# Performance work log

Hardware: AMD Instinct MI355X
Metric: run time of the kernel (lower is better)

Reference implementation:

```python
import jax, jax.numpy as jnp
import numpy as np

# dims (match init_kwargs)
N, M = 128, 2048
DX, DY, DU, DZ = 64, 8, 256, 256
EPS = 0.01


def setup_inputs() -> dict:
    key = jax.random.key(0)
    kit = iter(jax.random.split(key, 40))
    def w(*shape):
        fan_in = shape[-1]
        return jax.random.normal(next(kit), shape, jnp.float32) / np.float32(np.sqrt(fan_in))
    def b(*shape):
        return 0.1 * jax.random.normal(next(kit), shape, jnp.float32)
    inp = {
        'X_tensor': jax.random.normal(next(kit), (N, DX), jnp.float32),
        'U_tensor': jax.random.normal(next(kit), (M, DY), jnp.float32),
        'Y_tensor': jax.random.normal(next(kit), (N, DY), jnp.float32),
        # context path (x -> u_i)
        'Wt0': w(DU, DX), 'bt0': b(DU),
        'Wt1': w(DU, DU), 'bt1': b(DU),
        # PICNN cell 0 (input cell, no z term)
        'Wyu0': w(DY, DX), 'byu0': b(DY), 'Wy0': w(DZ, DY), 'Wu0': w(DZ, DX), 'b0': b(DZ),
        # PICNN cell 1 (hidden cell, nonneg Wz1 via softplus)
        'Wzu1': w(DZ, DU), 'bzu1': b(DZ), 'Wz1': w(DZ, DZ),
        'Wyu1': w(DY, DU), 'byu1': b(DY), 'Wy1': w(DZ, DY), 'Wu1': w(DZ, DU), 'b1': b(DZ),
        # PICNN cell 2 (output cell, scalar potential)
        'Wzu2': w(DZ, DU), 'bzu2': b(DZ), 'Wz2': w(1, DZ),
        'Wyu2': w(DY, DU), 'byu2': b(DY), 'Wy2': w(1, DY), 'Wu2': w(1, DU), 'b2': b(1),
    }
    return inp


def _psi(X, U, Y, Wt0, bt0, Wt1, bt1, Wyu0, byu0, Wy0, Wu0, b0,
         Wzu1, bzu1, Wz1, Wyu1, byu1, Wy1, Wu1, b1,
         Wzu2, bzu2, Wz2, Wyu2, byu2, Wy2, Wu2, b2):
    relu = jax.nn.relu
    # context path depends only on X -> compute once per row, broadcast over m samples
    u1 = relu(X @ Wt0.T + bt0)                       # [n, du]
    u2 = relu(u1 @ Wt1.T + bt1)                      # [n, du]
    # cell 0: z1 [n, m, dz]  (pairwise over X rows x U samples)
    gy0 = X @ Wyu0.T + byu0                          # [n, dy]
    z1 = relu(jnp.einsum('md,nd,zd->nmz', U, gy0, Wy0)
              + (X @ Wu0.T + b0)[:, None, :])
    # cell 1: hidden convex cell with nonneg z-weight
    gz1 = relu(u1 @ Wzu1.T + bzu1)                   # [n, dz]
    gy1 = u1 @ Wyu1.T + byu1                         # [n, dy]
    z2 = relu(jnp.einsum('nmz,nz,kz->nmk', z1, gz1, jax.nn.softplus(Wz1))
              + jnp.einsum('md,nd,kd->nmk', U, gy1, Wy1)
              + (u1 @ Wu1.T + b1)[:, None, :])       # [n, m, dz]
    # output cell -> scalar potential phi(x_i, u_j)
    gz2 = relu(u2 @ Wzu2.T + bzu2)                   # [n, dz]
    gy2 = u2 @ Wyu2.T + byu2                         # [n, dy]
    phi = (jnp.einsum('nmz,nz,z->nm', z2, gz2, jax.nn.softplus(Wz2)[0])
           + jnp.einsum('md,nd,d->nm', U, gy2, Wy2[0])
           + (u2 @ Wu2[0] + b2[0])[:, None])         # [n, m]
    # entropic OT dual psi with stable row-wise logsumexp
    cost = Y @ U.T                                   # [n, m]
    slack = cost - phi
    row_max = jnp.max(slack, axis=1, keepdims=True)
    log_mean_exp = (jax.nn.logsumexp((slack - row_max) / EPS, axis=1, keepdims=True)
                    - jnp.log(jnp.float32(slack.shape[1])))
    return EPS * (log_mean_exp + row_max / EPS)      # [n, 1]


def reference(X_tensor, U_tensor, Y_tensor, Wt0, bt0, Wt1, bt1, Wyu0, byu0, Wy0, Wu0, b0,
              Wzu1, bzu1, Wz1, Wyu1, byu1, Wy1, Wu1, b1,
              Wzu2, bzu2, Wz2, Wyu2, byu2, Wy2, Wu2, b2):
    return _psi(X_tensor, U_tensor, Y_tensor, Wt0, bt0, Wt1, bt1, Wyu0, byu0, Wy0, Wu0, b0,
                Wzu1, bzu1, Wz1, Wyu1, byu1, Wy1, Wu1, b1,
                Wzu2, bzu2, Wz2, Wyu2, byu2, Wy2, Wu2, b2)
```

## Files before the change

kernel.cpp:

```cpp
#include <hip/hip_runtime.h>

#define NN 128
#define MM 2048
#define EPSF 0.01f

typedef __bf16 bf16x8 __attribute__((ext_vector_type(8)));
typedef __bf16 bf16x4 __attribute__((ext_vector_type(4)));
typedef float  f32x4  __attribute__((ext_vector_type(4)));

#define WS_SLACK 0
#define WS_W2    262144
#define WS_GZ1   294912
#define WS_YV    327680
#define WS_CU2   328704
#define WS_WTF   328832
#define WS_A2    361600
#define WS_B2    394368
#define WS_BX    918656

__device__ __forceinline__ float softplusf(float x) {
    return x > 20.f ? x : log1pf(expf(x));
}

__device__ __forceinline__ bf16x8 ld_cvt8(const float* __restrict__ p) {
    const float4* p4 = (const float4*)p;
    float4 a = p4[0], b = p4[1];
    bf16x8 r;
    r[0] = (__bf16)a.x; r[1] = (__bf16)a.y; r[2] = (__bf16)a.z; r[3] = (__bf16)a.w;
    r[4] = (__bf16)b.x; r[5] = (__bf16)b.y; r[6] = (__bf16)b.z; r[7] = (__bf16)b.w;
    return r;
}

__global__ __launch_bounds__(256) void k_ctx3(
    const float* __restrict__ X, const float* __restrict__ Y,
    const float* __restrict__ U,
    const float* __restrict__ Wt0, const float* __restrict__ bt0,
    const float* __restrict__ Wt1, const float* __restrict__ bt1,
    const float* __restrict__ Wyu0, const float* __restrict__ byu0,
    const float* __restrict__ Wy0,
    const float* __restrict__ Wu0, const float* __restrict__ b0,
    const float* __restrict__ Wzu1, const float* __restrict__ bzu1,
    const float* __restrict__ Wz1,
    const float* __restrict__ Wyu1, const float* __restrict__ byu1,
    const float* __restrict__ Wy1,
    const float* __restrict__ Wu1, const float* __restrict__ b1,
    const float* __restrict__ Wzu2, const float* __restrict__ bzu2,
    const float* __restrict__ Wz2,
    const float* __restrict__ Wyu2, const float* __restrict__ byu2,
    const float* __restrict__ Wy2,
    const float* __restrict__ Wu2, const float* __restrict__ b2,
    float* __restrict__ ws)
{
    __shared__ __bf16 u1b[16][264];
    __shared__ __bf16 u2b[16][264];
    __shared__ __bf16 c0q[16][64];
    __shared__ __bf16 c1q[16][64];
    __shared__ float gy0s[16][8];
    __shared__ float gy1s[16][8];

    const int t = threadIdx.x, b = blockIdx.x;
    const int w = t >> 6, lane = t & 63;
    const int c = lane & 15, q = lane >> 4;
    const int g = b >> 2, s = b & 3;
    const int nb = g * 16;

#pragma unroll
    for (int jj = 0; jj < 2; ++jj) {
        const int o = (b * 512 + jj * 256 + t) * 4;
        const int j0 = o & 7;
        const int cc = (o >> 3) & 15;
        const int qq = (o >> 7) & 3;
        const int ch = (o >> 9) & 7;
        const int kt = o >> 12;
        const float* src = Wz1 + (kt * 16 + cc) * 256 + ch * 32 + qq * 8 + j0;
        float4 v = *(const float4*)src;
        bf16x4 r;
        r[0] = (__bf16)softplusf(v.x); r[1] = (__bf16)softplusf(v.y);
        r[2] = (__bf16)softplusf(v.z); r[3] = (__bf16)softplusf(v.w);
        *(bf16x4*)((__bf16*)(ws + WS_WTF) + o) = r;
    }
#pragma unroll
    for (int j = 0; j < 8; ++j) {
        const int i = b * 2048 + j * 256 + t;
        const int m = i >> 5, cc = i & 31;
        float v = cc < 8 ? U[m * 8 + cc] : (cc == 8 ? 1.f : 0.f);
        ((__bf16*)(ws + WS_A2))[i] = (__bf16)v;
    }

    bf16x8 a1[2];
#pragma unroll
    for (int ch = 0; ch < 2; ++ch)
        a1[ch] = ld_cvt8(X + (nb + c) * 64 + ch * 32 + q * 8);

    for (int tt = w; tt < 16; tt += 4) {
        const int col = tt * 16 + c;
        const float* rp = Wt0 + col * 64;
        f32x4 D = {0.f, 0.f, 0.f, 0.f};
#pragma unroll
        for (int ch = 0; ch < 2; ++ch) {
            bf16x8 bb = ld_cvt8(rp + ch * 32 + q * 8);
            D = __builtin_amdgcn_mfma_f32_16x16x32_bf16(a1[ch], bb, D, 0, 0, 0);
        }
        const float bv = bt0[col];
#pragma unroll
        for (int r = 0; r < 4; ++r)
            u1b[4 * q + r][col] = (__bf16)fmaxf(D[r] + bv, 0.f);
    }
    {
        const int col = (4 * s + w) * 16 + c;
        const float* rp = Wu0 + col * 64;
        f32x4 D = {0.f, 0.f, 0.f, 0.f};
#pragma unroll
        for (int ch = 0; ch < 2; ++ch) {
            bf16x8 bb = ld_cvt8(rp + ch * 32 + q * 8);
            D = __builtin_amdgcn_mfma_f32_16x16x32_bf16(a1[ch], bb, D, 0, 0, 0);
        }
        const float bv = b0[col];
#pragma unroll
        for (int r = 0; r < 4; ++r)
            c0q[4 * q + r][w * 16 + c] = (__bf16)(D[r] + bv);
    }
    if (w == 0) {
        const float* rp = Wyu0 + (c & 7) * 64;
        f32x4 D = {0.f, 0.f, 0.f, 0.f};
#pragma unroll
        for (int ch = 0; ch < 2; ++ch) {
            bf16x8 bb = ld_cvt8(rp + ch * 32 + q * 8);
            D = __builtin_amdgcn_mfma_f32_16x16x32_bf16(a1[ch], bb, D, 0, 0, 0);
        }
        if (c < 8) {
            const float bv = byu0[c];
#pragma unroll
            for (int r = 0; r < 4; ++r)
                gy0s[4 * q + r][c] = D[r] + bv;
        }
    }
    __syncthreads();

    bf16x8 aF[8];
#pragma unroll
    for (int ch = 0; ch < 8; ++ch)
        aF[ch] = *(const bf16x8*)&u1b[c][ch * 32 + q * 8];

    for (int tt = w; tt < 16; tt += 4) {
        const int col = tt * 16 + c;
        const float* rp = Wt1 + col * 256;
        f32x4 D = {0.f, 0.f, 0.f, 0.f};
#pragma unroll
        for (int ch = 0; ch < 8; ++ch) {
            bf16x8 bb = ld_cvt8(rp + ch * 32 + q * 8);
            D = __builtin_amdgcn_mfma_f32_16x16x32_bf16(aF[ch], bb, D, 0, 0, 0);
        }
        const float bv = bt1[col];
#pragma unroll
        for (int r = 0; r < 4; ++r)
            u2b[4 * q + r][col] = (__bf16)fmaxf(D[r] + bv, 0.f);
    }
    {
        const int col = (4 * s + w) * 16 + c;
        const float* rp = Wzu1 + col * 256;
        f32x4 D = {0.f, 0.f, 0.f, 0.f};
#pragma unroll
        for (int ch = 0; ch < 8; ++ch) {
            bf16x8 bb = ld_cvt8(rp + ch * 32 + q * 8);
            D = __builtin_amdgcn_mfma_f32_16x16x32_bf16(aF[ch], bb, D, 0, 0, 0);
        }
        const float bv = bzu1[col];
#pragma unroll
        for (int r = 0; r < 4; ++r)
            ws[WS_GZ1 + (nb + 4 * q + r) * 256 + col] = fmaxf(D[r] + bv, 0.f);
    }
    {
        const int col = (4 * s + w) * 16 + c;
        const float* rp = Wu1 + col * 256;
        f32x4 D = {0.f, 0.f, 0.f, 0.f};
#pragma unroll
        for (int ch = 0; ch < 8; ++ch) {
            bf16x8 bb = ld_cvt8(rp + ch * 32 + q * 8);
            D = __builtin_amdgcn_mfma_f32_16x16x32_bf16(aF[ch], bb, D, 0, 0, 0);
        }
        const float bv = b1[col];
#pragma unroll
        for (int r = 0; r < 4; ++r)
            c1q[4 * q + r][w * 16 + c] = (__bf16)(D[r] + bv);
    }
    if (w == 0) {
        const float* rp = Wyu1 + (c & 7) * 256;
        f32x4 D = {0.f, 0.f, 0.f, 0.f};
#pragma unroll
        for (int ch = 0; ch < 8; ++ch) {
            bf16x8 bb = ld_cvt8(rp + ch * 32 + q * 8);
            D = __builtin_amdgcn_mfma_f32_16x16x32_bf16(aF[ch], bb, D, 0, 0, 0);
        }
        if (c < 8) {
            const float bv = byu1[c];
#pragma unroll
            for (int r = 0; r < 4; ++r)
                gy1s[4 * q + r][c] = D[r] + bv;
        }
    }
    __syncthreads();

    bf16x8 aG[8];
#pragma unroll
    for (int ch = 0; ch < 8; ++ch)
        aG[ch] = *(const bf16x8*)&u2b[c][ch * 32 + q * 8];

    {
        const int col = (4 * s + w) * 16 + c;
        const float* rp = Wzu2 + col * 256;
        f32x4 D = {0.f, 0.f, 0.f, 0.f};
#pragma unroll
        for (int ch = 0; ch < 8; ++ch) {
            bf16x8 bb = ld_cvt8(rp + ch * 32 + q * 8);
            D = __builtin_amdgcn_mfma_f32_16x16x32_bf16(aG[ch], bb, D, 0, 0, 0);
        }
        const float bv = bzu2[col];
        const float sp = softplusf(Wz2[col]);
#pragma unroll
        for (int r = 0; r < 4; ++r) {
            float gz2 = fmaxf(D[r] + bv, 0.f);
            ws[WS_W2 + (nb + 4 * q + r) * 256 + col] = gz2 * sp;
        }
    }
    if (s == 0 && w == 0) {
        const float* rp = (c < 8) ? (Wyu2 + c * 256) : Wu2;
        f32x4 D = {0.f, 0.f, 0.f, 0.f};
#pragma unroll
        for (int ch = 0; ch < 8; ++ch) {
            bf16x8 bb = ld_cvt8(rp + ch * 32 + q * 8);
            D = __builtin_amdgcn_mfma_f32_16x16x32_bf16(aG[ch], bb, D, 0, 0, 0);
        }
        if (c < 8) {
            const float bv = byu2[c];
            const float wy2 = Wy2[c];
#pragma unroll
            for (int r = 0; r < 4; ++r) {
                const int n = nb + 4 * q + r;
                ws[WS_YV + n * 8 + c] = Y[n * 8 + c] - (D[r] + bv) * wy2;
            }
        } else if (c == 8) {
#pragma unroll
            for (int r = 0; r < 4; ++r)
                ws[WS_CU2 + nb + 4 * q + r] = D[r] + b2[0];
        }
    }

    bf16x8 zz;
#pragma unroll
    for (int j = 0; j < 8; ++j) zz[j] = (__bf16)0.f;
#pragma unroll
    for (int j = 0; j < 4; ++j) {
        const int idx = j * 256 + t;
        const int zl = idx & 63, nl = idx >> 6;
        const int z = 64 * s + zl, n = nb + nl;
        {
            const float* wy = Wy0 + z * 8;
            __bf16* dst = (__bf16*)(ws + WS_B2) + (n * 256 + z) * 32;
            bf16x8 v0, v1 = zz;
#pragma unroll
            for (int d = 0; d < 8; ++d) v0[d] = (__bf16)(gy0s[nl][d] * wy[d]);
            v1[0] = c0q[nl][zl];
            *(bf16x8*)(dst)      = v0;
            *(bf16x8*)(dst + 8)  = v1;
            *(bf16x8*)(dst + 16) = zz;
            *(bf16x8*)(dst + 24) = zz;
        }
        {
            const float* wy = Wy1 + z * 8;
            __bf16* dst = (__bf16*)(ws + WS_BX) + (n * 256 + z) * 32;
            bf16x8 v0, v1 = zz;
#pragma unroll
            for (int d = 0; d < 8; ++d) v0[d] = (__bf16)(gy1s[nl][d] * wy[d]);
            v1[0] = c1q[nl][zl];
            *(bf16x8*)(dst)      = v0;
            *(bf16x8*)(dst + 8)  = v1;
            *(bf16x8*)(dst + 16) = zz;
            *(bf16x8*)(dst + 24) = zz;
        }
    }
}

__global__ __launch_bounds__(256, 4) void k_main(
    const float* __restrict__ U,
    float* __restrict__ ws)
{
    __shared__ __bf16 zh[64][264];
    __shared__ float gz1s[256];
    __shared__ float w2s[256];
    __shared__ float sdot[64];
    __shared__ float psum[4][64];

    const int t  = threadIdx.x;
    const int n  = blockIdx.y;
    const int m0 = blockIdx.x * 64;
    const int w    = t >> 6;
    const int lane = t & 63;
    const int c = lane & 15;
    const int q = lane >> 4;

    gz1s[t] = ws[WS_GZ1 + n * 256 + t];
    w2s[t]  = ws[WS_W2  + n * 256 + t];
    if (t < 64) {
        float sd = 0.f;
#pragma unroll
        for (int d = 0; d < 8; ++d)
            sd += U[(m0 + t) * 8 + d] * ws[WS_YV + n * 8 + d];
        sdot[t] = sd;
    }

    const __bf16* A2p = (const __bf16*)(ws + WS_A2);
    const __bf16* B2p = (const __bf16*)(ws + WS_B2) + n * 8192;
    const __bf16* BXp = (const __bf16*)(ws + WS_BX) + n * 8192;
    const __bf16* WTF = (const __bf16*)(ws + WS_WTF);

    bf16x8 a2f[4];
#pragma unroll
    for (int mi = 0; mi < 4; ++mi)
        a2f[mi] = *(const bf16x8*)(A2p + (m0 + 16 * mi + c) * 32 + q * 8);

    {
        bf16x8 b2f[4];
#pragma unroll
        for (int zt = 0; zt < 4; ++zt)
            b2f[zt] = *(const bf16x8*)(B2p + (64 * w + 16 * zt + c) * 32 + q * 8);
        f32x4 pre[4][4];
#pragma unroll
        for (int zt = 0; zt < 4; ++zt)
#pragma unroll
            for (int mi = 0; mi < 4; ++mi) {
                f32x4 zacc = {0.f, 0.f, 0.f, 0.f};
                pre[zt][mi] = __builtin_amdgcn_mfma_f32_16x16x32_bf16(
                    b2f[zt], a2f[mi], zacc, 0, 0, 0);
            }
#pragma unroll
        for (int zt = 0; zt < 4; ++zt) {
            const int zb = 64 * w + 16 * zt + 4 * q;
#pragma unroll
            for (int mi = 0; mi < 4; ++mi) {
                bf16x4 v4;
#pragma unroll
                for (int r = 0; r < 4; ++r)
                    v4[r] = (__bf16)(fmaxf(pre[zt][mi][r], 0.f) * gz1s[zb + r]);
                *(bf16x4*)&zh[c + 16 * mi][zb] = v4;
            }
        }
    }

    f32x4 acc[4][4];
#pragma unroll
    for (int mi = 0; mi < 4; ++mi)
#pragma unroll
        for (int kj = 0; kj < 4; ++kj)
            acc[mi][kj] = f32x4{0.f, 0.f, 0.f, 0.f};

    __syncthreads();

    for (int ch = 0; ch < 8; ++ch) {
        bf16x8 az[4], bw[4];
#pragma unroll
        for (int mi = 0; mi < 4; ++mi)
            az[mi] = *(const bf16x8*)&zh[c + 16 * mi][ch * 32 + q * 8];
#pragma unroll
        for (int kj = 0; kj < 4; ++kj)
            bw[kj] = *(const bf16x8*)(WTF + ((4 * w + kj) * 8 + ch) * 512 + lane * 8);
#pragma unroll
        for (int mi = 0; mi < 4; ++mi)
#pragma unroll
            for (int kj = 0; kj < 4; ++kj)
                acc[mi][kj] = __builtin_amdgcn_mfma_f32_16x16x32_bf16(
                    az[mi], bw[kj], acc[mi][kj], 0, 0, 0);
    }
    {
        bf16x8 bx[4];
#pragma unroll
        for (int kj = 0; kj < 4; ++kj)
            bx[kj] = *(const bf16x8*)(BXp + (64 * w + 16 * kj + c) * 32 + q * 8);
#pragma unroll
        for (int mi = 0; mi < 4; ++mi)
#pragma unroll
            for (int kj = 0; kj < 4; ++kj)
                acc[mi][kj] = __builtin_amdgcn_mfma_f32_16x16x32_bf16(
                    a2f[mi], bx[kj], acc[mi][kj], 0, 0, 0);
    }

    float p[4][4];
#pragma unroll
    for (int mi = 0; mi < 4; ++mi)
#pragma unroll
        for (int r = 0; r < 4; ++r) p[mi][r] = 0.f;
#pragma unroll
    for (int kj = 0; kj < 4; ++kj) {
        float w2v = w2s[64 * w + 16 * kj + c];
#pragma unroll
        for (int mi = 0; mi < 4; ++mi)
#pragma unroll
            for (int r = 0; r < 4; ++r)
                p[mi][r] += fmaxf(acc[mi][kj][r], 0.f) * w2v;
    }
#pragma unroll
    for (int mi = 0; mi < 4; ++mi)
#pragma unroll
        for (int r = 0; r < 4; ++r) {
            float v = p[mi][r];
            v += __shfl_xor(v, 8);
            v += __shfl_xor(v, 4);
            v += __shfl_xor(v, 2);
            v += __shfl_xor(v, 1);
            p[mi][r] = v;
        }
    if (c == 0) {
#pragma unroll
        for (int mi = 0; mi < 4; ++mi)
            *(float4*)&psum[w][16 * mi + 4 * q] =
                make_float4(p[mi][0], p[mi][1], p[mi][2], p[mi][3]);
    }
    __syncthreads();
    if (t < 64) {
        float cu2 = ws[WS_CU2 + n];
        float pp = psum[0][t] + psum[1][t] + psum[2][t] + psum[3][t];
        ws[WS_SLACK + n * 2048 + m0 + t] = sdot[t] - cu2 - pp;
    }
}

__global__ __launch_bounds__(256) void k_lse(const float* __restrict__ ws,
                                             float* __restrict__ out) {
    __shared__ float redmax[4];
    __shared__ float redsum[4];
    const int n = blockIdx.x;
    const int t = threadIdx.x;
    const float* s = ws + WS_SLACK + n * 2048;

    float vals[8];
    float mx = -3.4e38f;
#pragma unroll
    for (int i = 0; i < 8; ++i) {
        vals[i] = s[t + 256 * i];
        mx = fmaxf(mx, vals[i]);
    }
#pragma unroll
    for (int off = 32; off; off >>= 1) mx = fmaxf(mx, __shfl_xor(mx, off));
    if ((t & 63) == 0) redmax[t >> 6] = mx;
    __syncthreads();
    mx = fmaxf(fmaxf(redmax[0], redmax[1]), fmaxf(redmax[2], redmax[3]));

    float sum = 0.f;
#pragma unroll
    for (int i = 0; i < 8; ++i) sum += expf((vals[i] - mx) * (1.f / EPSF));
#pragma unroll
    for (int off = 32; off; off >>= 1) sum += __shfl_xor(sum, off);
    if ((t & 63) == 0) redsum[t >> 6] = sum;
    __syncthreads();
    if (t == 0) {
        float S = redsum[0] + redsum[1] + redsum[2] + redsum[3];
        out[n] = EPSF * logf(S * (1.f / 2048.f)) + mx;
    }
}

extern "C" void kernel_launch(void* const* d_in, const int* in_sizes, int n_in,
                              void* d_out, int out_size, void* d_ws, size_t ws_size,
                              hipStream_t stream) {
    const float* X    = (const float*)d_in[0];
    const float* Uu   = (const float*)d_in[1];
    const float* Yy   = (const float*)d_in[2];
    const float* Wt0  = (const float*)d_in[3];
    const float* bt0  = (const float*)d_in[4];
    const float* Wt1  = (const float*)d_in[5];
    const float* bt1  = (const float*)d_in[6];
    const float* Wyu0 = (const float*)d_in[7];
    const float* byu0 = (const float*)d_in[8];
    const float* Wy0  = (const float*)d_in[9];
    const float* Wu0  = (const float*)d_in[10];
    const float* b0   = (const float*)d_in[11];
    const float* Wzu1 = (const float*)d_in[12];
    const float* bzu1 = (const float*)d_in[13];
    const float* Wz1  = (const float*)d_in[14];
    const float* Wyu1 = (const float*)d_in[15];
    const float* byu1 = (const float*)d_in[16];
    const float* Wy1  = (const float*)d_in[17];
    const float* Wu1  = (const float*)d_in[18];
    const float* b1   = (const float*)d_in[19];
    const float* Wzu2 = (const float*)d_in[20];
    const float* bzu2 = (const float*)d_in[21];
    const float* Wz2  = (const float*)d_in[22];
    const float* Wyu2 = (const float*)d_in[23];
    const float* byu2 = (const float*)d_in[24];
    const float* Wy2  = (const float*)d_in[25];
    const float* Wu2  = (const float*)d_in[26];
    const float* b2   = (const float*)d_in[27];
    float* ws  = (float*)d_ws;
    float* out = (float*)d_out;

    k_ctx3<<<dim3(32), dim3(256), 0, stream>>>(
        X, Yy, Uu, Wt0, bt0, Wt1, bt1, Wyu0, byu0, Wy0, Wu0, b0,
        Wzu1, bzu1, Wz1, Wyu1, byu1, Wy1, Wu1, b1,
        Wzu2, bzu2, Wz2, Wyu2, byu2, Wy2, Wu2, b2, ws);
    k_main<<<dim3(MM / 64, NN), dim3(256), 0, stream>>>(Uu, ws);
    k_lse<<<dim3(128), dim3(256), 0, stream>>>(ws, out);
}
```

Baseline: 183.9 us.

## Pre-convert weights to bf16 MFMA fragments in a separate wide kernel

```diff
diff --git a/kernel.cpp b/kernel.cpp
--- a/kernel.cpp
+++ b/kernel.cpp
@@ -9,6 +9,13 @@
 typedef float  f32x4  __attribute__((ext_vector_type(4)));
 
 #define WS_SLACK 0
+#define WS_WT1F  0
+#define WS_WZU1F 32768
+#define WS_WU1F  65536
+#define WS_WZU2F 98304
+#define WS_WT0F  131072
+#define WS_WU0F  139264
+#define WS_XF    147456
 #define WS_W2    262144
 #define WS_GZ1   294912
 #define WS_YV    327680
@@ -31,24 +38,81 @@
     return r;
 }
 
-__global__ __launch_bounds__(256) void k_ctx3(
-    const float* __restrict__ X, const float* __restrict__ Y,
-    const float* __restrict__ U,
-    const float* __restrict__ Wt0, const float* __restrict__ bt0,
-    const float* __restrict__ Wt1, const float* __restrict__ bt1,
+template<int CH, bool SP>
+__device__ __forceinline__ void frag_cvt(const float* __restrict__ W,
+                                         __bf16* __restrict__ F, int o) {
+    const int j0 = o & 7;
+    const int lane = (o >> 3) & 63;
+    const int c = lane & 15, q = lane >> 4;
+    const int ch = (o >> 9) & (CH - 1);
+    const int ot = o >> (CH == 8 ? 12 : 10);
+    const float* src = W + (ot * 16 + c) * (CH * 32) + ch * 32 + q * 8 + j0;
+    float4 v = *(const float4*)src;
+    bf16x4 r;
+    if (SP) {
+        r[0] = (__bf16)softplusf(v.x); r[1] = (__bf16)softplusf(v.y);
+        r[2] = (__bf16)softplusf(v.z); r[3] = (__bf16)softplusf(v.w);
+    } else {
+        r[0] = (__bf16)v.x; r[1] = (__bf16)v.y;
+        r[2] = (__bf16)v.z; r[3] = (__bf16)v.w;
+    }
+    *(bf16x4*)(F + o) = r;
+}
+
+__global__ __launch_bounds__(256) void k_wprep(
+    const float* __restrict__ X, const float* __restrict__ U,
+    const float* __restrict__ Wt0, const float* __restrict__ Wu0,
+    const float* __restrict__ Wt1, const float* __restrict__ Wzu1,
+    const float* __restrict__ Wu1, const float* __restrict__ Wzu2,
+    const float* __restrict__ Wz1,
+    float* __restrict__ ws)
+{
+    const int b = blockIdx.x, t = threadIdx.x;
+    if (b < 64) {
+        frag_cvt<8, true>(Wz1, (__bf16*)(ws + WS_WTF), b * 1024 + t * 4);
+    } else if (b < 128) {
+        const int i = (b - 64) * 1024 + t * 4;
+        const int m = i >> 5, cc = i & 31;
+        bf16x4 r;
+        if (cc < 8) {
+            float4 u = *(const float4*)(U + m * 8 + cc);
+            r[0] = (__bf16)u.x; r[1] = (__bf16)u.y;
+            r[2] = (__bf16)u.z; r[3] = (__bf16)u.w;
+        } else if (cc == 8) {
+            r[0] = (__bf16)1.f; r[1] = (__bf16)0.f; r[2] = (__bf16)0.f; r[3] = (__bf16)0.f;
+        } else {
+            r[0] = (__bf16)0.f; r[1] = (__bf16)0.f; r[2] = (__bf16)0.f; r[3] = (__bf16)0.f;
+        }
+        *(bf16x4*)((__bf16*)(ws + WS_A2) + i) = r;
+    } else if (b < 192) {
+        frag_cvt<8, false>(Wt1, (__bf16*)(ws + WS_WT1F), (b - 128) * 1024 + t * 4);
+    } else if (b < 256) {
+        frag_cvt<8, false>(Wzu1, (__bf16*)(ws + WS_WZU1F), (b - 192) * 1024 + t * 4);
+    } else if (b < 320) {
+        frag_cvt<8, false>(Wu1, (__bf16*)(ws + WS_WU1F), (b - 256) * 1024 + t * 4);
+    } else if (b < 384) {
+        frag_cvt<8, false>(Wzu2, (__bf16*)(ws + WS_WZU2F), (b - 320) * 1024 + t * 4);
+    } else if (b < 400) {
+        frag_cvt<2, false>(Wt0, (__bf16*)(ws + WS_WT0F), (b - 384) * 1024 + t * 4);
+    } else if (b < 416) {
+        frag_cvt<2, false>(Wu0, (__bf16*)(ws + WS_WU0F), (b - 400) * 1024 + t * 4);
+    } else {
+        frag_cvt<2, false>(X, (__bf16*)(ws + WS_XF), (b - 416) * 1024 + t * 4);
+    }
+}
+
+__global__ __launch_bounds__(512) void k_ctx4(
+    const float* __restrict__ Y,
+    const float* __restrict__ bt0, const float* __restrict__ b0,
     const float* __restrict__ Wyu0, const float* __restrict__ byu0,
     const float* __restrict__ Wy0,
-    const float* __restrict__ Wu0, const float* __restrict__ b0,
-    const float* __restrict__ Wzu1, const float* __restrict__ bzu1,
-    const float* __restrict__ Wz1,
+    const float* __restrict__ bt1, const float* __restrict__ bzu1,
     const float* __restrict__ Wyu1, const float* __restrict__ byu1,
     const float* __restrict__ Wy1,
-    const float* __restrict__ Wu1, const float* __restrict__ b1,
-    const float* __restrict__ Wzu2, const float* __restrict__ bzu2,
-    const float* __restrict__ Wz2,
+    const float* __restrict__ b1,
+    const float* __restrict__ bzu2, const float* __restrict__ Wz2,
     const float* __restrict__ Wyu2, const float* __restrict__ byu2,
-    const float* __restrict__ Wy2,
-    const float* __restrict__ Wu2, const float* __restrict__ b2,
+    const float* __restrict__ Wy2, const float* __restrict__ b2,
     float* __restrict__ ws)
 {
     __shared__ __bf16 u1b[16][264];
@@ -64,70 +128,51 @@
     const int g = b >> 2, s = b & 3;
     const int nb = g * 16;
 
-#pragma unroll
-    for (int jj = 0; jj < 2; ++jj) {
-        const int o = (b * 512 + jj * 256 + t) * 4;
-        const int j0 = o & 7;
-        const int cc = (o >> 3) & 15;
-        const int qq = (o >> 7) & 3;
-        const int ch = (o >> 9) & 7;
-        const int kt = o >> 12;
-        const float* src = Wz1 + (kt * 16 + cc) * 256 + ch * 32 + qq * 8 + j0;
-        float4 v = *(const float4*)src;
-        bf16x4 r;
-        r[0] = (__bf16)softplusf(v.x); r[1] = (__bf16)softplusf(v.y);
-        r[2] = (__bf16)softplusf(v.z); r[3] = (__bf16)softplusf(v.w);
-        *(bf16x4*)((__bf16*)(ws + WS_WTF) + o) = r;
-    }
-#pragma unroll
-    for (int j = 0; j < 8; ++j) {
-        const int i = b * 2048 + j * 256 + t;
-        const int m = i >> 5, cc = i & 31;
-        float v = cc < 8 ? U[m * 8 + cc] : (cc == 8 ? 1.f : 0.f);
-        ((__bf16*)(ws + WS_A2))[i] = (__bf16)v;
-    }
+    const __bf16* Xf    = (const __bf16*)(ws + WS_XF);
+    const __bf16* Wt0f  = (const __bf16*)(ws + WS_WT0F);
+    const __bf16* Wu0f  = (const __bf16*)(ws + WS_WU0F);
+    const __bf16* Wt1f  = (const __bf16*)(ws + WS_WT1F);
+    const __bf16* Wzu1f = (const __bf16*)(ws + WS_WZU1F);
+    const __bf16* Wu1f  = (const __bf16*)(ws + WS_WU1F);
+    const __bf16* Wzu2f = (const __bf16*)(ws + WS_WZU2F);
 
     bf16x8 a1[2];
 #pragma unroll
     for (int ch = 0; ch < 2; ++ch)
-        a1[ch] = ld_cvt8(X + (nb + c) * 64 + ch * 32 + q * 8);
-
-    for (int tt = w; tt < 16; tt += 4) {
-        const int col = tt * 16 + c;
-        const float* rp = Wt0 + col * 64;
+        a1[ch] = *(const bf16x8*)(Xf + ((g * 2 + ch) * 64 + lane) * 8);
+
+    for (int tt = w; tt < 16; tt += 8) {
+        f32x4 D = {0.f, 0.f, 0.f, 0.f};
+#pragma unroll
+        for (int ch = 0; ch < 2; ++ch) {
+            bf16x8 bb = *(const bf16x8*)(Wt0f + ((tt * 2 + ch) * 64 + lane) * 8);
+            D = __builtin_amdgcn_mfma_f32_16x16x32_bf16(a1[ch], bb, D, 0, 0, 0);
+        }
+        const float bv = bt0[tt * 16 + c];
+#pragma unroll
+        for (int r = 0; r < 4; ++r)
+            u1b[4 * q + r][tt * 16 + c] = (__bf16)fmaxf(D[r] + bv, 0.f);
+    }
+    if (w < 4) {
+        const int ot = 4 * s + w;
+        f32x4 D = {0.f, 0.f, 0.f, 0.f};
+#pragma unroll
+        for (int ch = 0; ch < 2; ++ch) {
+            bf16x8 bb = *(const bf16x8*)(Wu0f + ((ot * 2 + ch) * 64 + lane) * 8);
+            D = __builtin_amdgcn_mfma_f32_16x16x32_bf16(a1[ch], bb, D, 0, 0, 0);
+        }
+        const float bv = b0[ot * 16 + c];
+#pragma unroll
+        for (int r = 0; r < 4; ++r)
+            c0q[4 * q + r][w * 16 + c] = (__bf16)(D[r] + bv);
+    } else if (w == 4) {
+        const float* rp = Wyu0 + (c & 7) * 64;
         f32x4 D = {0.f, 0.f, 0.f, 0.f};
 #pragma unroll
         for (int ch = 0; ch < 2; ++ch) {
             bf16x8 bb = ld_cvt8(rp + ch * 32 + q * 8);
             D = __builtin_amdgcn_mfma_f32_16x16x32_bf16(a1[ch], bb, D, 0, 0, 0);
         }
-        const float bv = bt0[col];
-#pragma unroll
-        for (int r = 0; r < 4; ++r)
-            u1b[4 * q + r][col] = (__bf16)fmaxf(D[r] + bv, 0.f);
-    }
-    {
-        const int col = (4 * s + w) * 16 + c;
-        const float* rp = Wu0 + col * 64;
-        f32x4 D = {0.f, 0.f, 0.f, 0.f};
-#pragma unroll
-        for (int ch = 0; ch < 2; ++ch) {
-            bf16x8 bb = ld_cvt8(rp + ch * 32 + q * 8);
-            D = __builtin_amdgcn_mfma_f32_16x16x32_bf16(a1[ch], bb, D, 0, 0, 0);
-        }
-        const float bv = b0[col];
-#pragma unroll
-        for (int r = 0; r < 4; ++r)
-            c0q[4 * q + r][w * 16 + c] = (__bf16)(D[r] + bv);
-    }
-    if (w == 0) {
-        const float* rp = Wyu0 + (c & 7) * 64;
-        f32x4 D = {0.f, 0.f, 0.f, 0.f};
-#pragma unroll
-        for (int ch = 0; ch < 2; ++ch) {
-            bf16x8 bb = ld_cvt8(rp + ch * 32 + q * 8);
-            D = __builtin_amdgcn_mfma_f32_16x16x32_bf16(a1[ch], bb, D, 0, 0, 0);
-        }
         if (c < 8) {
             const float bv = byu0[c];
 #pragma unroll
@@ -142,56 +187,51 @@
     for (int ch = 0; ch < 8; ++ch)
         aF[ch] = *(const bf16x8*)&u1b[c][ch * 32 + q * 8];
 
-    for (int tt = w; tt < 16; tt += 4) {
-        const int col = tt * 16 + c;
-        const float* rp = Wt1 + col * 256;
+    for (int tt = w; tt < 16; tt += 8) {
+        f32x4 D = {0.f, 0.f, 0.f, 0.f};
+#pragma unroll
+        for (int ch = 0; ch < 8; ++ch) {
+            bf16x8 bb = *(const bf16x8*)(Wt1f + ((tt * 8 + ch) * 64 + lane) * 8);
+            D = __builtin_amdgcn_mfma_f32_16x16x32_bf16(aF[ch], bb, D, 0, 0, 0);
+        }
+        const float bv = bt1[tt * 16 + c];
+#pragma unroll
+        for (int r = 0; r < 4; ++r)
+            u2b[4 * q + r][tt * 16 + c] = (__bf16)fmaxf(D[r] + bv, 0.f);
+    }
+    if (w < 4) {
+        const int ot = 4 * s + w, col = ot * 16 + c;
+        f32x4 D = {0.f, 0.f, 0.f, 0.f};
+#pragma unroll
+        for (int ch = 0; ch < 8; ++ch) {
+            bf16x8 bb = *(const bf16x8*)(Wzu1f + ((ot * 8 + ch) * 64 + lane) * 8);
+            D = __builtin_amdgcn_mfma_f32_16x16x32_bf16(aF[ch], bb, D, 0, 0, 0);
+        }
+        const float bv = bzu1[col];
+#pragma unroll
+        for (int r = 0; r < 4; ++r)
+            ws[WS_GZ1 + (nb + 4 * q + r) * 256 + col] = fmaxf(D[r] + bv, 0.f);
+    } else {
+        const int ot = 4 * s + (w - 4);
+        f32x4 D = {0.f, 0.f, 0.f, 0.f};
+#pragma unroll
+        for (int ch = 0; ch < 8; ++ch) {
+            bf16x8 bb = *(const bf16x8*)(Wu1f + ((ot * 8 + ch) * 64 + lane) * 8);
+            D = __builtin_amdgcn_mfma_f32_16x16x32_bf16(aF[ch], bb, D, 0, 0, 0);
+        }
+        const float bv = b1[ot * 16 + c];
+#pragma unroll
+        for (int r = 0; r < 4; ++r)
+            c1q[4 * q + r][(w - 4) * 16 + c] = (__bf16)(D[r] + bv);
+    }
+    if (w == 0) {
+        const float* rp = Wyu1 + (c & 7) * 256;
         f32x4 D = {0.f, 0.f, 0.f, 0.f};
 #pragma unroll
         for (int ch = 0; ch < 8; ++ch) {
             bf16x8 bb = ld_cvt8(rp + ch * 32 + q * 8);
             D = __builtin_amdgcn_mfma_f32_16x16x32_bf16(aF[ch], bb, D, 0, 0, 0);
         }
-        const float bv = bt1[col];
-#pragma unroll
-        for (int r = 0; r < 4; ++r)
-            u2b[4 * q + r][col] = (__bf16)fmaxf(D[r] + bv, 0.f);
-    }
-    {
-        const int col = (4 * s + w) * 16 + c;
-        const float* rp = Wzu1 + col * 256;
-        f32x4 D = {0.f, 0.f, 0.f, 0.f};
-#pragma unroll
-        for (int ch = 0; ch < 8; ++ch) {
-            bf16x8 bb = ld_cvt8(rp + ch * 32 + q * 8);
-            D = __builtin_amdgcn_mfma_f32_16x16x32_bf16(aF[ch], bb, D, 0, 0, 0);
-        }
-        const float bv = bzu1[col];
-#pragma unroll
-        for (int r = 0; r < 4; ++r)
-            ws[WS_GZ1 + (nb + 4 * q + r) * 256 + col] = fmaxf(D[r] + bv, 0.f);
-    }
-    {
-        const int col = (4 * s + w) * 16 + c;
-        const float* rp = Wu1 + col * 256;
-        f32x4 D = {0.f, 0.f, 0.f, 0.f};
-#pragma unroll
-        for (int ch = 0; ch < 8; ++ch) {
-            bf16x8 bb = ld_cvt8(rp + ch * 32 + q * 8);
-            D = __builtin_amdgcn_mfma_f32_16x16x32_bf16(aF[ch], bb, D, 0, 0, 0);
-        }
-        const float bv = b1[col];
-#pragma unroll
-        for (int r = 0; r < 4; ++r)
-            c1q[4 * q + r][w * 16 + c] = (__bf16)(D[r] + bv);
-    }
-    if (w == 0) {
-        const float* rp = Wyu1 + (c & 7) * 256;
-        f32x4 D = {0.f, 0.f, 0.f, 0.f};
-#pragma unroll
-        for (int ch = 0; ch < 8; ++ch) {
-            bf16x8 bb = ld_cvt8(rp + ch * 32 + q * 8);
-            D = __builtin_amdgcn_mfma_f32_16x16x32_bf16(aF[ch], bb, D, 0, 0, 0);
-        }
         if (c < 8) {
             const float bv = byu1[c];
 #pragma unroll
@@ -206,13 +246,12 @@
     for (int ch = 0; ch < 8; ++ch)
         aG[ch] = *(const bf16x8*)&u2b[c][ch * 32 + q * 8];
 
-    {
-        const int col = (4 * s + w) * 16 + c;
-        const float* rp = Wzu2 + col * 256;
+    if (w < 4) {
+        const int ot = 4 * s + w, col = ot * 16 + c;
         f32x4 D = {0.f, 0.f, 0.f, 0.f};
 #pragma unroll
         for (int ch = 0; ch < 8; ++ch) {
-            bf16x8 bb = ld_cvt8(rp + ch * 32 + q * 8);
+            bf16x8 bb = *(const bf16x8*)(Wzu2f + ((ot * 8 + ch) * 64 + lane) * 8);
             D = __builtin_amdgcn_mfma_f32_16x16x32_bf16(aG[ch], bb, D, 0, 0, 0);
         }
         const float bv = bzu2[col];
@@ -222,64 +261,66 @@
             float gz2 = fmaxf(D[r] + bv, 0.f);
             ws[WS_W2 + (nb + 4 * q + r) * 256 + col] = gz2 * sp;
         }
-    }
-    if (s == 0 && w == 0) {
-        const float* rp = (c < 8) ? (Wyu2 + c * 256) : Wu2;
-        f32x4 D = {0.f, 0.f, 0.f, 0.f};
-#pragma unroll
-        for (int ch = 0; ch < 8; ++ch) {
-            bf16x8 bb = ld_cvt8(rp + ch * 32 + q * 8);
-            D = __builtin_amdgcn_mfma_f32_16x16x32_bf16(aG[ch], bb, D, 0, 0, 0);
-        }
-        if (c < 8) {
-            const float bv = byu2[c];
-            const float wy2 = Wy2[c];
-#pragma unroll
-            for (int r = 0; r < 4; ++r) {
-                const int n = nb + 4 * q + r;
-                ws[WS_YV + n * 8 + c] = Y[n * 8 + c] - (D[r] + bv) * wy2;
+    } else if (w == 4 && s == 0) {
+        const float* rp = (c < 8) ? (Wyu2 + c * 256) : Wyu2;
+        if (c >= 8) rp = (const float*)Wz2;
+        rp = (c < 8) ? (Wyu2 + c * 256) : ((const float*)0);
+        ;
+        f32x4 D = {0.f, 0.f, 0.f, 0.f};
+        const float* rpp = (c < 8) ? (Wyu2 + c * 256) : (byu2 - byu2 + (const float*)nullptr);
+        (void)rp; (void)rpp;
+        D = f32x4{0.f, 0.f, 0.f, 0.f};
+        const float* rr = (c < 8) ? (Wyu2 + c * 256) : nullptr;
+        (void)rr;
+        ;
+    }
+    if (w == 4 && s == 0) {
+        extern const float* __yv_dummy;
+    }
+    {
+    }
+    if (w == 5 && s == 0) { }
+
+    if (w == 4 && s == 0) {
+    }
+
+    {
+        bf16x8 zz;
+#pragma unroll
+        for (int j = 0; j < 8; ++j) zz[j] = (__bf16)0.f;
+#pragma unroll
+        for (int j = 0; j < 2; ++j) {
+            const int idx = j * 512 + t;
+            const int zl = idx & 63, nl = idx >> 6;
+            const int z = 64 * s + zl, n = nb + nl;
+            {
+                const float* wy = Wy0 + z * 8;
+                __bf16* dst = (__bf16*)(ws + WS_B2) + (n * 256 + z) * 32;
+                bf16x8 v0, v1 = zz;
+#pragma unroll
+                for (int d = 0; d < 8; ++d) v0[d] = (__bf16)(gy0s[nl][d] * wy[d]);
+                v1[0] = c0q[nl][zl];
+                *(bf16x8*)(dst)      = v0;
+                *(bf16x8*)(dst + 8)  = v1;
+                *(bf16x8*)(dst + 16) = zz;
+                *(bf16x8*)(dst + 24) = zz;
             }
-        } else if (c == 8) {
-#pragma unroll
-            for (int r = 0; r < 4; ++r)
-                ws[WS_CU2 + nb + 4 * q + r] = D[r] + b2[0];
-        }
-    }
-
-    bf16x8 zz;
-#pragma unroll
-    for (int j = 0; j < 8; ++j) zz[j] = (__bf16)0.f;
-#pragma unroll
-    for (int j = 0; j < 4; ++j) {
-        const int idx = j * 256 + t;
-        const int zl = idx & 63, nl = idx >> 6;
-        const int z = 64 * s + zl, n = nb + nl;
-        {
-            const float* wy = Wy0 + z * 8;
-            __bf16* dst = (__bf16*)(ws + WS_B2) + (n * 256 + z) * 32;
-            bf16x8 v0, v1 = zz;
-#pragma unroll
-            for (int d = 0; d < 8; ++d) v0[d] = (__bf16)(gy0s[nl][d] * wy[d]);
-            v1[0] = c0q[nl][zl];
-            *(bf16x8*)(dst)      = v0;
-            *(bf16x8*)(dst + 8)  = v1;
-            *(bf16x8*)(dst + 16) = zz;
-            *(bf16x8*)(dst + 24) = zz;
-        }
-        {
-            const float* wy = Wy1 + z * 8;
-            __bf16* dst = (__bf16*)(ws + WS_BX) + (n * 256 + z) * 32;
-            bf16x8 v0, v1 = zz;
-#pragma unroll
-            for (int d = 0; d < 8; ++d) v0[d] = (__bf16)(gy1s[nl][d] * wy[d]);
-            v1[0] = c1q[nl][zl];
-            *(bf16x8*)(dst)      = v0;
-            *(bf16x8*)(dst + 8)  = v1;
-            *(bf16x8*)(dst + 16) = zz;
-            *(bf16x8*)(dst + 24) = zz;
-        }
-    }
-}
+            {
+                const float* wy = Wy1 + z * 8;
+                __bf16* dst = (__bf16*)(ws + WS_BX) + (n * 256 + z) * 32;
+                bf16x8 v0, v1 = zz;
+#pragma unroll
+                for (int d = 0; d < 8; ++d) v0[d] = (__bf16)(gy1s[nl][d] * wy[d]);
+                v1[0] = c1q[nl][zl];
+                *(bf16x8*)(dst)      = v0;
+                *(bf16x8*)(dst + 8)  = v1;
+                *(bf16x8*)(dst + 16) = zz;
+                *(bf16x8*)(dst + 24) = zz;
+            }
+        }
+    }
+}
+
 
 __global__ __launch_bounds__(256, 4) void k_main(
     const float* __restrict__ U,
@@ -454,6 +495,89 @@
     if (t == 0) {
         float S = redsum[0] + redsum[1] + redsum[2] + redsum[3];
         out[n] = EPSF * logf(S * (1.f / 2048.f)) + mx;
+    }
+}
+
+__global__ __launch_bounds__(256) void k_yvcu(
+    const float* __restrict__ Y,
+    const float* __restrict__ bt0, const float* __restrict__ bt1,
+    const float* __restrict__ Wyu2, const float* __restrict__ byu2,
+    const float* __restrict__ Wy2,
+    const float* __restrict__ Wu2, const float* __restrict__ b2,
+    float* __restrict__ ws)
+{
+    __shared__ __bf16 u1b[16][264];
+    __shared__ __bf16 u2b[16][264];
+    const int t = threadIdx.x, g = blockIdx.x;
+    const int w = t >> 6, lane = t & 63;
+    const int c = lane & 15, q = lane >> 4;
+    const int nb = g * 16;
+
+    const __bf16* Xf   = (const __bf16*)(ws + WS_XF);
+    const __bf16* Wt0f = (const __bf16*)(ws + WS_WT0F);
+    const __bf16* Wt1f = (const __bf16*)(ws + WS_WT1F);
+
+    bf16x8 a1[2];
+#pragma unroll
+    for (int ch = 0; ch < 2; ++ch)
+        a1[ch] = *(const bf16x8*)(Xf + ((g * 2 + ch) * 64 + lane) * 8);
+    for (int tt = w; tt < 16; tt += 4) {
+        f32x4 D = {0.f, 0.f, 0.f, 0.f};
+#pragma unroll
+        for (int ch = 0; ch < 2; ++ch) {
+            bf16x8 bb = *(const bf16x8*)(Wt0f + ((tt * 2 + ch) * 64 + lane) * 8);
+            D = __builtin_amdgcn_mfma_f32_16x16x32_bf16(a1[ch], bb, D, 0, 0, 0);
+        }
+        const float bv = bt0[tt * 16 + c];
+#pragma unroll
+        for (int r = 0; r < 4; ++r)
+            u1b[4 * q + r][tt * 16 + c] = (__bf16)fmaxf(D[r] + bv, 0.f);
+    }
+    __syncthreads();
+
+    bf16x8 aF[8];
+#pragma unroll
+    for (int ch = 0; ch < 8; ++ch)
+        aF[ch] = *(const bf16x8*)&u1b[c][ch * 32 + q * 8];
+    for (int tt = w; tt < 16; tt += 4) {
+        f32x4 D = {0.f, 0.f, 0.f, 0.f};
+#pragma unroll
+        for (int ch = 0; ch < 8; ++ch) {
+            bf16x8 bb = *(const bf16x8*)(Wt1f + ((tt * 8 + ch) * 64 + lane) * 8);
+            D = __builtin_amdgcn_mfma_f32_16x16x32_bf16(aF[ch], bb, D, 0, 0, 0);
+        }
+        const float bv = bt1[tt * 16 + c];
+#pragma unroll
+        for (int r = 0; r < 4; ++r)
+            u2b[4 * q + r][tt * 16 + c] = (__bf16)fmaxf(D[r] + bv, 0.f);
+    }
+    __syncthreads();
+
+    if (w == 0) {
+        bf16x8 aG[8];
+#pragma unroll
+        for (int ch = 0; ch < 8; ++ch)
+            aG[ch] = *(const bf16x8*)&u2b[c][ch * 32 + q * 8];
+        const float* rp = (c < 8) ? (Wyu2 + c * 256) : Wu2;
+        f32x4 D = {0.f, 0.f, 0.f, 0.f};
+#pragma unroll
+        for (int ch = 0; ch < 8; ++ch) {
+            bf16x8 bb = ld_cvt8(rp + ch * 32 + q * 8);
+            D = __builtin_amdgcn_mfma_f32_16x16x32_bf16(aG[ch], bb, D, 0, 0, 0);
+        }
+        if (c < 8) {
+            const float bv = byu2[c];
+            const float wy2 = Wy2[c];
+#pragma unroll
+            for (int r = 0; r < 4; ++r) {
+                const int n = nb + 4 * q + r;
+                ws[WS_YV + n * 8 + c] = Y[n * 8 + c] - (D[r] + bv) * wy2;
+            }
+        } else if (c == 8) {
+#pragma unroll
+            for (int r = 0; r < 4; ++r)
+                ws[WS_CU2 + nb + 4 * q + r] = D[r] + b2[0];
+        }
     }
 }
 
@@ -491,10 +615,13 @@
     float* ws  = (float*)d_ws;
     float* out = (float*)d_out;
 
-    k_ctx3<<<dim3(32), dim3(256), 0, stream>>>(
-        X, Yy, Uu, Wt0, bt0, Wt1, bt1, Wyu0, byu0, Wy0, Wu0, b0,
-        Wzu1, bzu1, Wz1, Wyu1, byu1, Wy1, Wu1, b1,
-        Wzu2, bzu2, Wz2, Wyu2, byu2, Wy2, Wu2, b2, ws);
+    k_wprep<<<dim3(424), dim3(256), 0, stream>>>(
+        X, Uu, Wt0, Wu0, Wt1, Wzu1, Wu1, Wzu2, Wz1, ws);
+    k_ctx4<<<dim3(32), dim3(512), 0, stream>>>(
+        Yy, bt0, b0, Wyu0, byu0, Wy0, bt1, bzu1, Wyu1, byu1, Wy1, b1,
+        bzu2, Wz2, Wyu2, byu2, Wy2, b2, ws);
+    k_yvcu<<<dim3(8), dim3(256), 0, stream>>>(
+        Yy, bt0, bt1, Wyu2, byu2, Wy2, Wu2, b2, ws);
     k_main<<<dim3(MM / 64, NN), dim3(256), 0, stream>>>(Uu, ws);
     k_lse<<<dim3(128), dim3(256), 0, stream>>>(ws, out);
 }
```

New measurement: 176.4 us. -4.1%, faster.
